# Kernel tuning notes

Hardware: AMD Instinct MI355X
Metric: run time of the kernel (lower is better)

Reference implementation:

```python
import jax, jax.numpy as jnp
import numpy as np

N_HEAD = 16
NEG_BIG = 1e10


def setup_inputs() -> dict:
    key = jax.random.key(0)
    ks = jax.random.split(key, 4)
    B, T, D = 2, 2048, 1024
    x = jax.random.normal(ks[0], (B, T, D), dtype=jnp.float32)
    w_attn = jax.random.normal(ks[1], (D, 3 * D), dtype=jnp.float32) * 0.02
    b_attn = jnp.zeros((3 * D,), dtype=jnp.float32)
    w_proj = jax.random.normal(ks[2], (D, D), dtype=jnp.float32) * 0.02
    b_proj = jnp.zeros((D,), dtype=jnp.float32)
    return {"x": x, "w_attn": w_attn, "b_attn": b_attn, "w_proj": w_proj, "b_proj": b_proj}


def reference(x, w_attn, b_attn, w_proj, b_proj):
    B, T, D = x.shape
    H = N_HEAD
    dh = D // H
    # fused QKV projection (Conv1d == addmm: x @ W + b)
    qkv = x @ w_attn + b_attn                      # [B, T, 3D]
    q, k, v = jnp.split(qkv, 3, axis=-1)
    # split heads -> [B, H, T, dh]
    q = q.reshape(B, T, H, dh).transpose(0, 2, 1, 3)
    k = k.reshape(B, T, H, dh).transpose(0, 2, 1, 3)
    v = v.reshape(B, T, H, dh).transpose(0, 2, 1, 3)
    # scores; repo scales by 1/sqrt(n_head) (its idiosyncrasy, kept faithfully)
    w = jnp.einsum('bhqd,bhkd->bhqk', q, k) / jnp.sqrt(jnp.float32(H))
    # causal mask via repo formula: w*b - 1e10*(1-b), b = tril ones
    b = jnp.tril(jnp.ones((T, T), dtype=w.dtype))
    w = w * b - NEG_BIG * (1.0 - b)
    w = jax.nn.softmax(w, axis=-1)
    a = jnp.einsum('bhqk,bhkd->bhqd', w, v)        # [B, H, T, dh]
    # merge heads
    a = a.transpose(0, 2, 1, 3).reshape(B, T, D)
    a = a @ w_proj + b_proj
    present = jnp.stack([k, v])                     # [2, B, H, T, dh]
    return a, present
```

## Files before the change

kernel.cpp:

```cpp
#include <hip/hip_runtime.h>
#include <hip/hip_bf16.h>

typedef __hip_bfloat16 bf16;
typedef unsigned short ush;
typedef __attribute__((ext_vector_type(8))) short bf16x8;
typedef __attribute__((ext_vector_type(4))) float f32x4;

#define BB 2
#define TT 2048
#define DD 1024
#define HH 16
#define DHH 64
#define MM (BB*TT)
#define N3 (3*DD)

__device__ __forceinline__ bf16  f2b(float x){ return __float2bfloat16(x); }
__device__ __forceinline__ ush   f2bu(float x){ bf16 h = __float2bfloat16(x); return *(ush*)&h; }

#define GLOAD_LDS(gp, lp) \
    __builtin_amdgcn_global_load_lds( \
        (const __attribute__((address_space(1))) void*)(gp), \
        (__attribute__((address_space(3))) void*)(lp), 16, 0, 0)

__global__ __launch_bounds__(256) void prep_fused(
    const float* __restrict__ x, const float* __restrict__ w_attn,
    ush* __restrict__ xbf, ush* __restrict__ wT)
{
    __shared__ ush T[64][68];
    const int tid = threadIdx.x;
    const int bid = blockIdx.x;

    if (bid < 2048) {
        const size_t i = ((size_t)bid * 256 + tid) * 8;
        float4 a = *(const float4*)&x[i];
        float4 b = *(const float4*)&x[i + 4];
        ushort4 u0; u0.x = f2bu(a.x); u0.y = f2bu(a.y); u0.z = f2bu(a.z); u0.w = f2bu(a.w);
        ushort4 u1; u1.x = f2bu(b.x); u1.y = f2bu(b.y); u1.z = f2bu(b.z); u1.w = f2bu(b.w);
        *(ushort4*)&xbf[i] = u0;
        *(ushort4*)&xbf[i + 4] = u1;
        return;
    }
    const int j  = bid - 2048;
    const int c0 = (j % 48) * 64;
    const int r0 = (j / 48) * 64;
    #pragma unroll
    for (int it = 0; it < 4; it++) {
        int idx = it * 256 + tid;
        int i = idx >> 4, jf = idx & 15;
        float4 v = *(const float4*)&w_attn[(size_t)(r0 + i) * N3 + c0 + jf * 4];
        T[jf * 4 + 0][i] = f2bu(v.x);
        T[jf * 4 + 1][i] = f2bu(v.y);
        T[jf * 4 + 2][i] = f2bu(v.z);
        T[jf * 4 + 3][i] = f2bu(v.w);
    }
    __syncthreads();
    #pragma unroll
    for (int it = 0; it < 4; it++) {
        int idx = it * 256 + tid;
        int jj = idx >> 4, i4 = idx & 15;
        *(ushort4*)&wT[(size_t)(c0 + jj) * DD + r0 + i4 * 4] =
            *(const ushort4*)&T[jj][i4 * 4];
    }
}

__global__ __launch_bounds__(256) void transpose_cvt(
    const float* __restrict__ src, ush* __restrict__ dst, int R, int C)
{
    __shared__ ush T[64][68];
    const int tid = threadIdx.x;
    const int c0 = blockIdx.x * 64;
    const int r0 = blockIdx.y * 64;

    #pragma unroll
    for (int it = 0; it < 4; it++) {
        int idx = it * 256 + tid;
        int i = idx >> 4, jf = idx & 15;
        float4 v = *(const float4*)&src[(size_t)(r0 + i) * C + c0 + jf * 4];
        T[jf * 4 + 0][i] = f2bu(v.x);
        T[jf * 4 + 1][i] = f2bu(v.y);
        T[jf * 4 + 2][i] = f2bu(v.z);
        T[jf * 4 + 3][i] = f2bu(v.w);
    }
    __syncthreads();
    #pragma unroll
    for (int it = 0; it < 4; it++) {
        int idx = it * 256 + tid;
        int j = idx >> 4, i4 = idx & 15;
        *(ushort4*)&dst[(size_t)(c0 + j) * R + r0 + i4 * 4] =
            *(const ushort4*)&T[j][i4 * 4];
    }
}

__global__ __launch_bounds__(256) void qkv_mfma(
    const ush* __restrict__ xbf, const ush* __restrict__ wT,
    const float* __restrict__ bias,
    bf16* __restrict__ qws, float* __restrict__ kout, float* __restrict__ vout,
    ush* __restrict__ kbf, ush* __restrict__ vtb, int write_bf)
{
    __shared__ __align__(16) ush As[128 * 32];
    __shared__ __align__(16) ush Bs[128 * 32];

    const int tid  = threadIdx.x;
    const int lane = tid & 63;
    const int w    = tid >> 6;
    const int n16  = lane & 15;
    const int quad = lane >> 4;
    const int row0 = blockIdx.y * 128;
    const int col0 = blockIdx.x * 128;
    const int wrow = (w >> 1) * 64;
    const int wcol = (w & 1) * 64;

    f32x4 acc[4][4];
    #pragma unroll
    for (int mb = 0; mb < 4; mb++)
        #pragma unroll
        for (int nb = 0; nb < 4; nb++) acc[mb][nb] = (f32x4){0.f,0.f,0.f,0.f};

    for (int kk0 = 0; kk0 < DD; kk0 += 32) {
        __syncthreads();
        #pragma unroll
        for (int it = 0; it < 2; it++) {
            int c = it * 256 + tid;
            int r = c >> 2, co = (c & 3) * 8;
            GLOAD_LDS(&xbf[(size_t)(row0 + r) * DD + kk0 + co], &As[c * 8]);
            GLOAD_LDS(&wT[(size_t)(col0 + r) * DD + kk0 + co], &Bs[c * 8]);
        }
        __syncthreads();

        bf16x8 af[4];
        #pragma unroll
        for (int mb = 0; mb < 4; mb++)
            af[mb] = *(const bf16x8*)&As[(wrow + mb * 16 + n16) * 32 + quad * 8];
        #pragma unroll
        for (int nb = 0; nb < 4; nb++) {
            bf16x8 bfr = *(const bf16x8*)&Bs[(wcol + nb * 16 + n16) * 32 + quad * 8];
            #pragma unroll
            for (int mb = 0; mb < 4; mb++)
                acc[mb][nb] = __builtin_amdgcn_mfma_f32_16x16x32_bf16(
                    af[mb], bfr, acc[mb][nb], 0, 0, 0);
        }
    }

    const float qsc = write_bf ? 0.36067376022224085f : 1.0f;

    #pragma unroll
    for (int nb = 0; nb < 4; nb++) {
        const int gc = col0 + wcol + nb * 16 + n16;
        const float bv = bias[gc];
        const int which = gc >> 10;
        const int h = (gc & 1023) >> 6;
        const int d = gc & 63;
        #pragma unroll
        for (int mb = 0; mb < 4; mb++) {
            float vv[4];
            #pragma unroll
            for (int reg = 0; reg < 4; reg++) vv[reg] = acc[mb][nb][reg] + bv;
            const int gr0 = row0 + wrow + mb * 16 + quad * 4;
            const int b_ = gr0 >> 11, t0 = gr0 & 2047;
            const int bh = b_ * HH + h;
            const size_t tbase = ((size_t)bh * TT + t0) * DHH + d;
            if (which == 0) {
                #pragma unroll
                for (int reg = 0; reg < 4; reg++)
                    qws[tbase + (size_t)reg * DHH] = f2b(vv[reg] * qsc);
            } else if (which == 1) {
                if (write_bf) {
                    #pragma unroll
                    for (int reg = 0; reg < 4; reg++)
                        __builtin_nontemporal_store(vv[reg], &kout[tbase + (size_t)reg * DHH]);
                    #pragma unroll
                    for (int reg = 0; reg < 4; reg++)
                        kbf[tbase + (size_t)reg * DHH] = f2bu(vv[reg]);
                } else {
                    #pragma unroll
                    for (int reg = 0; reg < 4; reg++)
                        kout[tbase + (size_t)reg * DHH] = vv[reg];
                }
            } else {
                if (write_bf) {
                    #pragma unroll
                    for (int reg = 0; reg < 4; reg++)
                        __builtin_nontemporal_store(vv[reg], &vout[tbase + (size_t)reg * DHH]);
                    ushort4 u;
                    u.x = f2bu(vv[0]); u.y = f2bu(vv[1]);
                    u.z = f2bu(vv[2]); u.w = f2bu(vv[3]);
                    *(ushort4*)&vtb[((size_t)bh * DHH + d) * TT + t0] = u;
                } else {
                    #pragma unroll
                    for (int reg = 0; reg < 4; reg++)
                        vout[tbase + (size_t)reg * DHH] = vv[reg];
                }
            }
        }
    }
}

__global__ __launch_bounds__(256) void flash_attn_v6(
    const ush* __restrict__ qin, const ush* __restrict__ kbf,
    const ush* __restrict__ vtb, bf16* __restrict__ attn)
{
    __shared__ __align__(16) ush Ks[64][72];
    __shared__ __align__(16) ush Vt[64][72];

    const int tid  = threadIdx.x;
    const int lane = tid & 63;
    const int w    = tid >> 6;
    const int n16  = lane & 15;
    const int quad = lane >> 4;
    const int bh = blockIdx.y;
    const int qi = (bh & 8) ? (31 - (int)blockIdx.x) : (int)blockIdx.x;
    const int q0 = qi * 64;
    const ush* Qb  = qin + (size_t)bh * TT * DHH;
    const ush* Kb  = kbf + (size_t)bh * TT * DHH;
    const ush* Vtb = vtb + (size_t)bh * DHH * TT;
    const int b_ = bh >> 4, h = bh & 15;

    const ush* Qp = Qb + (size_t)(q0 + w * 16 + n16) * DHH + quad * 8;
    const bf16x8 qa0 = *(const bf16x8*)&Qp[0];
    const bf16x8 qa1 = *(const bf16x8*)&Qp[32];

    const int r0c = tid >> 3, c8c = (tid & 7) * 8;
    const int r1c = (256 + tid) >> 3, c8c1 = ((256 + tid) & 7) * 8;

    const int rsb = ((n16 >> 2) << 3) + ((n16 & 1) << 2) + ((n16 & 2) << 4);
    const int rq  = w * 16 + n16;

    bf16x8 kst[2], vst[2];
    {
        const ush* Kp = Kb;
        const ush* Vp = Vtb;
        kst[0] = *(const bf16x8*)&Kp[(size_t)r0c * DHH + c8c];
        kst[1] = *(const bf16x8*)&Kp[(size_t)r1c * DHH + c8c1];
        vst[0] = *(const bf16x8*)&Vp[(size_t)r0c * TT + c8c];
        vst[1] = *(const bf16x8*)&Vp[(size_t)r1c * TT + c8c1];
    }

    f32x4 o[4];
    #pragma unroll
    for (int db = 0; db < 4; db++) o[db] = (f32x4){0.f, 0.f, 0.f, 0.f};
    float lsum = 0.f;

    for (int kt = 0; kt <= qi; kt++) {
        __syncthreads();
        *(bf16x8*)&Ks[r0c][c8c]  = kst[0];
        *(bf16x8*)&Ks[r1c][c8c1] = kst[1];
        *(bf16x8*)&Vt[r0c][c8c]  = vst[0];
        *(bf16x8*)&Vt[r1c][c8c1] = vst[1];
        __syncthreads();

        if (kt < qi) {
            const ush* Kp = Kb + (size_t)((kt + 1) * 64) * DHH;
            const ush* Vp = Vtb + (kt + 1) * 64;
            kst[0] = *(const bf16x8*)&Kp[(size_t)r0c * DHH + c8c];
            kst[1] = *(const bf16x8*)&Kp[(size_t)r1c * DHH + c8c1];
            vst[0] = *(const bf16x8*)&Vp[(size_t)r0c * TT + c8c];
            vst[1] = *(const bf16x8*)&Vp[(size_t)r1c * TT + c8c1];
        }

        f32x4 s[4];
        #pragma unroll
        for (int m = 0; m < 4; m++) {
            bf16x8 kb0 = *(const bf16x8*)&Ks[rsb + m][quad * 8];
            bf16x8 kb1 = *(const bf16x8*)&Ks[rsb + m][32 + quad * 8];
            f32x4 a4 = (f32x4){0.f, 0.f, 0.f, 0.f};
            a4 = __builtin_amdgcn_mfma_f32_16x16x32_bf16(kb0, qa0, a4, 0, 0, 0);
            a4 = __builtin_amdgcn_mfma_f32_16x16x32_bf16(kb1, qa1, a4, 0, 0, 0);
            s[m] = a4;
        }

        float p[4][4];
        if (kt == qi) {
            #pragma unroll
            for (int m = 0; m < 4; m++) {
                #pragma unroll
                for (int reg = 0; reg < 4; reg++) {
                    const int kl = quad * 8 + m + ((reg & 1) << 2) + ((reg >> 1) << 5);
                    float pv = exp2f(s[m][reg]);
                    if (kl > rq) pv = 0.f;
                    p[m][reg] = pv;
                    lsum += pv;
                }
            }
        } else {
            #pragma unroll
            for (int m = 0; m < 4; m++) {
                #pragma unroll
                for (int reg = 0; reg < 4; reg++) {
                    float pv = exp2f(s[m][reg]);
                    p[m][reg] = pv;
                    lsum += pv;
                }
            }
        }

        bf16x8 pa0, pa1;
        #pragma unroll
        for (int m = 0; m < 4; m++) {
            pa0[m]     = (short)f2bu(p[m][0]);
            pa0[m + 4] = (short)f2bu(p[m][1]);
            pa1[m]     = (short)f2bu(p[m][2]);
            pa1[m + 4] = (short)f2bu(p[m][3]);
        }

        #pragma unroll
        for (int db = 0; db < 4; db++) {
            bf16x8 vb0 = *(const bf16x8*)&Vt[db * 16 + n16][quad * 8];
            bf16x8 vb1 = *(const bf16x8*)&Vt[db * 16 + n16][32 + quad * 8];
            o[db] = __builtin_amdgcn_mfma_f32_16x16x32_bf16(pa0, vb0, o[db], 0, 0, 0);
            o[db] = __builtin_amdgcn_mfma_f32_16x16x32_bf16(pa1, vb1, o[db], 0, 0, 0);
        }
    }

    float ls = lsum;
    ls += __shfl_xor(ls, 16);
    ls += __shfl_xor(ls, 32);
    #pragma unroll
    for (int reg = 0; reg < 4; reg++) {
        const float il = 1.0f / __shfl(ls, quad * 4 + reg);
        const int t_ = q0 + w * 16 + quad * 4 + reg;
        bf16* outr = attn + ((size_t)(b_ * TT + t_)) * DD + h * 64 + n16;
        #pragma unroll
        for (int db = 0; db < 4; db++)
            outr[db * 16] = f2b(o[db][reg] * il);
    }
}

__global__ __launch_bounds__(256) void flash_attn_mfma(
    const bf16* __restrict__ qin, const float* __restrict__ kin,
    const float* __restrict__ vin, bf16* __restrict__ attn)
{
    __shared__ __align__(16) ush Qs[64][72];
    __shared__ __align__(16) ush Ks[64][72];
    __shared__ __align__(16) ush Vt[64][72];
    __shared__ __align__(16) ush Ps[4][16][72];

    const int tid  = threadIdx.x;
    const int lane = tid & 63;
    const int w    = tid >> 6;
    const int n16  = lane & 15;
    const int quad = lane >> 4;
    const int qi = blockIdx.x;
    const int bh = blockIdx.y;
    const int q0 = qi * 64;

    const ush*   Qp = (const ush*)qin + ((size_t)bh * TT + q0) * DHH;
    const float* Kb = kin + (size_t)bh * TT * DHH;
    const float* Vb = vin + (size_t)bh * TT * DHH;

    #pragma unroll
    for (int it = 0; it < 4; it++) {
        int idx = (it * 256 + tid) * 4;
        int r = idx >> 6, d = idx & 63;
        *(ushort4*)&Qs[r][d] = *(const ushort4*)&Qp[idx];
    }

    f32x4 o[4];
    #pragma unroll
    for (int db = 0; db < 4; db++) o[db] = (f32x4){0.f, 0.f, 0.f, 0.f};
    float m_old[4] = {-1e30f, -1e30f, -1e30f, -1e30f};
    float l_run[4] = {0.f, 0.f, 0.f, 0.f};

    for (int kt = 0; kt <= qi; kt++) {
        const float* Kp = Kb + (size_t)(kt * 64) * DHH;
        const float* Vp = Vb + (size_t)(kt * 64) * DHH;
        __syncthreads();
        #pragma unroll
        for (int it = 0; it < 4; it++) {
            int idx = (it * 256 + tid) * 4;
            int c = idx >> 6, d = idx & 63;
            float4 kv = *(const float4*)&Kp[idx];
            ushort4 kb;
            kb.x = f2bu(kv.x); kb.y = f2bu(kv.y); kb.z = f2bu(kv.z); kb.w = f2bu(kv.w);
            *(ushort4*)&Ks[c][d] = kb;
        }
        #pragma unroll
        for (int it = 0; it < 4; it++) {
            int c = tid & 63, d0 = (tid >> 6) * 4 + it * 16;
            float4 vv = *(const float4*)&Vp[c * 64 + d0];
            Vt[d0 + 0][c] = f2bu(vv.x);
            Vt[d0 + 1][c] = f2bu(vv.y);
            Vt[d0 + 2][c] = f2bu(vv.z);
            Vt[d0 + 3][c] = f2bu(vv.w);
        }
        __syncthreads();

        bf16x8 qa0 = *(const bf16x8*)&Qs[w * 16 + n16][quad * 8];
        bf16x8 qa1 = *(const bf16x8*)&Qs[w * 16 + n16][32 + quad * 8];
        f32x4 s[4];
        #pragma unroll
        for (int cb = 0; cb < 4; cb++) {
            bf16x8 kb0 = *(const bf16x8*)&Ks[cb * 16 + n16][quad * 8];
            bf16x8 kb1 = *(const bf16x8*)&Ks[cb * 16 + n16][32 + quad * 8];
            f32x4 acc = (f32x4){0.f, 0.f, 0.f, 0.f};
            acc = __builtin_amdgcn_mfma_f32_16x16x32_bf16(qa0, kb0, acc, 0, 0, 0);
            acc = __builtin_amdgcn_mfma_f32_16x16x32_bf16(qa1, kb1, acc, 0, 0, 0);
            s[cb] = acc;
        }

        const int grow_base = q0 + w * 16 + quad * 4;
        const int gcol_base = kt * 64 + n16;
        #pragma unroll
        for (int reg = 0; reg < 4; reg++) {
            float sv[4];
            float pm = -1e30f;
            #pragma unroll
            for (int cb = 0; cb < 4; cb++) {
                float v = s[cb][reg] * 0.25f;
                if (gcol_base + cb * 16 > grow_base + reg) v = -1e10f;
                sv[cb] = v;
                pm = fmaxf(pm, v);
            }
            #pragma unroll
            for (int off = 1; off < 16; off <<= 1)
                pm = fmaxf(pm, __shfl_xor(pm, off));
            float mnew = fmaxf(m_old[reg], pm);
            float alpha = __expf(m_old[reg] - mnew);
            float ps = 0.f;
            #pragma unroll
            for (int cb = 0; cb < 4; cb++) {
                float p = __expf(sv[cb] - mnew);
                Ps[w][quad * 4 + reg][cb * 16 + n16] = f2bu(p);
                ps += p;
            }
            #pragma unroll
            for (int off = 1; off < 16; off <<= 1)
                ps += __shfl_xor(ps, off);
            l_run[reg] = l_run[reg] * alpha + ps;
            m_old[reg] = mnew;
            #pragma unroll
            for (int db = 0; db < 4; db++) o[db][reg] *= alpha;
        }
        __syncthreads();

        bf16x8 pa0 = *(const bf16x8*)&Ps[w][n16][quad * 8];
        bf16x8 pa1 = *(const bf16x8*)&Ps[w][n16][32 + quad * 8];
        #pragma unroll
        for (int db = 0; db < 4; db++) {
            bf16x8 vb0 = *(const bf16x8*)&Vt[db * 16 + n16][quad * 8];
            bf16x8 vb1 = *(const bf16x8*)&Vt[db * 16 + n16][32 + quad * 8];
            o[db] = __builtin_amdgcn_mfma_f32_16x16x32_bf16(pa0, vb0, o[db], 0, 0, 0);
            o[db] = __builtin_amdgcn_mfma_f32_16x16x32_bf16(pa1, vb1, o[db], 0, 0, 0);
        }
    }

    const int b_ = bh >> 4, h = bh & 15;
    #pragma unroll
    for (int reg = 0; reg < 4; reg++) {
        const float il = 1.0f / l_run[reg];
        const int t_ = q0 + w * 16 + quad * 4 + reg;
        bf16* outr = attn + ((size_t)(b_ * TT + t_)) * DD + h * 64 + n16;
        #pragma unroll
        for (int db = 0; db < 4; db++)
            outr[db * 16] = f2b(o[db][reg] * il);
    }
}

__global__ __launch_bounds__(256) void proj_mfma(
    const ush* __restrict__ a, const ush* __restrict__ wpT,
    const float* __restrict__ bias, float* __restrict__ out)
{
    __shared__ __align__(16) ush As[128 * 32];
    __shared__ __align__(16) ush Bs[128 * 32];

    const int tid  = threadIdx.x;
    const int lane = tid & 63;
    const int w    = tid >> 6;
    const int n16  = lane & 15;
    const int quad = lane >> 4;
    const int row0 = blockIdx.y * 128;
    const int col0 = blockIdx.x * 128;
    const int wrow = (w >> 1) * 64;
    const int wcol = (w & 1) * 64;

    f32x4 acc[4][4];
    #pragma unroll
    for (int mb = 0; mb < 4; mb++)
        #pragma unroll
        for (int nb = 0; nb < 4; nb++) acc[mb][nb] = (f32x4){0.f,0.f,0.f,0.f};

    for (int kk0 = 0; kk0 < DD; kk0 += 32) {
        __syncthreads();
        #pragma unroll
        for (int it = 0; it < 2; it++) {
            int c = it * 256 + tid;
            int r = c >> 2, co = (c & 3) * 8;
            GLOAD_LDS(&a[(size_t)(row0 + r) * DD + kk0 + co], &As[c * 8]);
            GLOAD_LDS(&wpT[(size_t)(col0 + r) * DD + kk0 + co], &Bs[c * 8]);
        }
        __syncthreads();

        bf16x8 af[4];
        #pragma unroll
        for (int mb = 0; mb < 4; mb++)
            af[mb] = *(const bf16x8*)&As[(wrow + mb * 16 + n16) * 32 + quad * 8];
        #pragma unroll
        for (int nb = 0; nb < 4; nb++) {
            bf16x8 bfr = *(const bf16x8*)&Bs[(wcol + nb * 16 + n16) * 32 + quad * 8];
            #pragma unroll
            for (int mb = 0; mb < 4; mb++)
                acc[mb][nb] = __builtin_amdgcn_mfma_f32_16x16x32_bf16(
                    af[mb], bfr, acc[mb][nb], 0, 0, 0);
        }
    }

    #pragma unroll
    for (int nb = 0; nb < 4; nb++) {
        const int gc = col0 + wcol + nb * 16 + n16;
        const float bv = bias[gc];
        #pragma unroll
        for (int mb = 0; mb < 4; mb++) {
            #pragma unroll
            for (int reg = 0; reg < 4; reg++) {
                const int gr = row0 + wrow + mb * 16 + quad * 4 + reg;
                __builtin_nontemporal_store(acc[mb][nb][reg] + bv,
                                            &out[(size_t)gr * DD + gc]);
            }
        }
    }
}

extern "C" void kernel_launch(void* const* d_in, const int* in_sizes, int n_in,
                              void* d_out, int out_size, void* d_ws, size_t ws_size,
                              hipStream_t stream) {
    const float *x = nullptr, *w_attn = nullptr, *b_attn = nullptr,
                *w_proj = nullptr, *b_proj = nullptr;
    for (int i = 0; i < n_in; i++) {
        switch (in_sizes[i]) {
            case 4194304: x      = (const float*)d_in[i]; break;
            case 3145728: w_attn = (const float*)d_in[i]; break;
            case 3072:    b_attn = (const float*)d_in[i]; break;
            case 1048576: w_proj = (const float*)d_in[i]; break;
            case 1024:    b_proj = (const float*)d_in[i]; break;
            default: break;
        }
    }
    if (!x || !w_attn || !b_attn || !w_proj || !b_proj) return;

    float* out_a = (float*)d_out;
    float* out_k = out_a + (size_t)MM * DD;
    float* out_v = out_k + (size_t)BB * HH * TT * DHH;

    const size_t MB = 1024 * 1024;
    char* wsc = (char*)d_ws;
    ush*  wT     = (ush*)(wsc + 0);
    bf16* attnws = (bf16*)(wsc + 0);
    bf16* qws    = (bf16*)(wsc + 8 * MB);
    ush*  wpT    = (ush*)(wsc + 8 * MB);
    ush*  xbf    = (ush*)d_out;

    if (ws_size >= 32 * MB) {
        ush* kbf = (ush*)(wsc + 16 * MB);
        ush* vtb = (ush*)(wsc + 24 * MB);
        prep_fused<<<dim3(2048 + 768), 256, 0, stream>>>(x, w_attn, xbf, wT);
        qkv_mfma<<<dim3(N3 / 128, MM / 128), 256, 0, stream>>>(
            xbf, wT, b_attn, qws, out_k, out_v, kbf, vtb, 1);
        flash_attn_v6<<<dim3(TT / 64, BB * HH), 256, 0, stream>>>(
            (const ush*)qws, kbf, vtb, attnws);
        transpose_cvt<<<dim3(DD / 64, DD / 64), 256, 0, stream>>>(w_proj, wpT, DD, DD);
        proj_mfma<<<dim3(DD / 128, MM / 128), 256, 0, stream>>>(
            (const ush*)attnws, wpT, b_proj, out_a);
    } else if (ws_size >= 16 * MB) {
        prep_fused<<<dim3(2048 + 768), 256, 0, stream>>>(x, w_attn, xbf, wT);
        qkv_mfma<<<dim3(N3 / 128, MM / 128), 256, 0, stream>>>(
            xbf, wT, b_attn, qws, out_k, out_v, nullptr, nullptr, 0);
        flash_attn_mfma<<<dim3(TT / 64, BB * HH), 256, 0, stream>>>(
            qws, out_k, out_v, attnws);
        transpose_cvt<<<dim3(DD / 64, DD / 64), 256, 0, stream>>>(w_proj, wpT, DD, DD);
        proj_mfma<<<dim3(DD / 128, MM / 128), 256, 0, stream>>>(
            (const ush*)attnws, wpT, b_proj, out_a);
    }
}
```

Before: 197.6 us.

## Double-buffer K/V tiles in flash attention and narrow projection GEMM tiles

The attention kernel now keeps two LDS buffers for K and V. The next tile is stored while the current one is computed, and the tile after that is prefetched into registers, so each iteration needs one barrier instead of two. The output projection GEMM drops from 128x128 to 128x64 tiles. That doubles the block count from 256 to 512 to fill more CUs, at the cost of more redundant A-tile loads. Its output stores also change from nontemporal to regular stores.

Measured after the change: 194.3 us. Within noise of the previous version (-1.7%).

```diff
diff --git a/kernel.cpp b/kernel.cpp
--- a/kernel.cpp
+++ b/kernel.cpp
@@ -195,12 +195,12 @@
     }
 }
 
-__global__ __launch_bounds__(256) void flash_attn_v6(
+__global__ __launch_bounds__(256) void flash_attn_v7(
     const ush* __restrict__ qin, const ush* __restrict__ kbf,
     const ush* __restrict__ vtb, bf16* __restrict__ attn)
 {
-    __shared__ __align__(16) ush Ks[64][72];
-    __shared__ __align__(16) ush Vt[64][72];
+    __shared__ __align__(16) ush Ks[2][64][72];
+    __shared__ __align__(16) ush Vt[2][64][72];
 
     const int tid  = threadIdx.x;
     const int lane = tid & 63;
@@ -226,42 +226,41 @@
     const int rq  = w * 16 + n16;
 
     bf16x8 kst[2], vst[2];
-    {
-        const ush* Kp = Kb;
-        const ush* Vp = Vtb;
-        kst[0] = *(const bf16x8*)&Kp[(size_t)r0c * DHH + c8c];
-        kst[1] = *(const bf16x8*)&Kp[(size_t)r1c * DHH + c8c1];
-        vst[0] = *(const bf16x8*)&Vp[(size_t)r0c * TT + c8c];
-        vst[1] = *(const bf16x8*)&Vp[(size_t)r1c * TT + c8c1];
-    }
+#define LOAD_TILE(kt) do { \
+        const ush* Kp_ = Kb + (size_t)((kt) * 64) * DHH; \
+        const ush* Vp_ = Vtb + (kt) * 64; \
+        kst[0] = *(const bf16x8*)&Kp_[(size_t)r0c * DHH + c8c]; \
+        kst[1] = *(const bf16x8*)&Kp_[(size_t)r1c * DHH + c8c1]; \
+        vst[0] = *(const bf16x8*)&Vp_[(size_t)r0c * TT + c8c]; \
+        vst[1] = *(const bf16x8*)&Vp_[(size_t)r1c * TT + c8c1]; \
+    } while(0)
+#define STORE_TILE(b) do { \
+        *(bf16x8*)&Ks[b][r0c][c8c]  = kst[0]; \
+        *(bf16x8*)&Ks[b][r1c][c8c1] = kst[1]; \
+        *(bf16x8*)&Vt[b][r0c][c8c]  = vst[0]; \
+        *(bf16x8*)&Vt[b][r1c][c8c1] = vst[1]; \
+    } while(0)
 
     f32x4 o[4];
     #pragma unroll
     for (int db = 0; db < 4; db++) o[db] = (f32x4){0.f, 0.f, 0.f, 0.f};
     float lsum = 0.f;
 
+    LOAD_TILE(0);
+    STORE_TILE(0);
+    if (qi > 0) LOAD_TILE(1);
+    __syncthreads();
+    int c = 0;
+
     for (int kt = 0; kt <= qi; kt++) {
-        __syncthreads();
-        *(bf16x8*)&Ks[r0c][c8c]  = kst[0];
-        *(bf16x8*)&Ks[r1c][c8c1] = kst[1];
-        *(bf16x8*)&Vt[r0c][c8c]  = vst[0];
-        *(bf16x8*)&Vt[r1c][c8c1] = vst[1];
-        __syncthreads();
-
-        if (kt < qi) {
-            const ush* Kp = Kb + (size_t)((kt + 1) * 64) * DHH;
-            const ush* Vp = Vtb + (kt + 1) * 64;
-            kst[0] = *(const bf16x8*)&Kp[(size_t)r0c * DHH + c8c];
-            kst[1] = *(const bf16x8*)&Kp[(size_t)r1c * DHH + c8c1];
-            vst[0] = *(const bf16x8*)&Vp[(size_t)r0c * TT + c8c];
-            vst[1] = *(const bf16x8*)&Vp[(size_t)r1c * TT + c8c1];
-        }
+        if (kt < qi) STORE_TILE(c ^ 1);
+        if (kt + 2 <= qi) LOAD_TILE(kt + 2);
 
         f32x4 s[4];
         #pragma unroll
         for (int m = 0; m < 4; m++) {
-            bf16x8 kb0 = *(const bf16x8*)&Ks[rsb + m][quad * 8];
-            bf16x8 kb1 = *(const bf16x8*)&Ks[rsb + m][32 + quad * 8];
+            bf16x8 kb0 = *(const bf16x8*)&Ks[c][rsb + m][quad * 8];
+            bf16x8 kb1 = *(const bf16x8*)&Ks[c][rsb + m][32 + quad * 8];
             f32x4 a4 = (f32x4){0.f, 0.f, 0.f, 0.f};
             a4 = __builtin_amdgcn_mfma_f32_16x16x32_bf16(kb0, qa0, a4, 0, 0, 0);
             a4 = __builtin_amdgcn_mfma_f32_16x16x32_bf16(kb1, qa1, a4, 0, 0, 0);
@@ -304,11 +303,14 @@
 
         #pragma unroll
         for (int db = 0; db < 4; db++) {
-            bf16x8 vb0 = *(const bf16x8*)&Vt[db * 16 + n16][quad * 8];
-            bf16x8 vb1 = *(const bf16x8*)&Vt[db * 16 + n16][32 + quad * 8];
+            bf16x8 vb0 = *(const bf16x8*)&Vt[c][db * 16 + n16][quad * 8];
+            bf16x8 vb1 = *(const bf16x8*)&Vt[c][db * 16 + n16][32 + quad * 8];
             o[db] = __builtin_amdgcn_mfma_f32_16x16x32_bf16(pa0, vb0, o[db], 0, 0, 0);
             o[db] = __builtin_amdgcn_mfma_f32_16x16x32_bf16(pa1, vb1, o[db], 0, 0, 0);
         }
+
+        __syncthreads();
+        c ^= 1;
     }
 
     float ls = lsum;
@@ -323,6 +325,8 @@
         for (int db = 0; db < 4; db++)
             outr[db * 16] = f2b(o[db][reg] * il);
     }
+#undef LOAD_TILE
+#undef STORE_TILE
 }
 
 __global__ __launch_bounds__(256) void flash_attn_mfma(
@@ -460,7 +464,7 @@
     const float* __restrict__ bias, float* __restrict__ out)
 {
     __shared__ __align__(16) ush As[128 * 32];
-    __shared__ __align__(16) ush Bs[128 * 32];
+    __shared__ __align__(16) ush Bs[64 * 32];
 
     const int tid  = threadIdx.x;
     const int lane = tid & 63;
@@ -468,15 +472,15 @@
     const int n16  = lane & 15;
     const int quad = lane >> 4;
     const int row0 = blockIdx.y * 128;
-    const int col0 = blockIdx.x * 128;
+    const int col0 = blockIdx.x * 64;
     const int wrow = (w >> 1) * 64;
-    const int wcol = (w & 1) * 64;
-
-    f32x4 acc[4][4];
+    const int wcol = (w & 1) * 32;
+
+    f32x4 acc[4][2];
     #pragma unroll
     for (int mb = 0; mb < 4; mb++)
         #pragma unroll
-        for (int nb = 0; nb < 4; nb++) acc[mb][nb] = (f32x4){0.f,0.f,0.f,0.f};
+        for (int nb = 0; nb < 2; nb++) acc[mb][nb] = (f32x4){0.f,0.f,0.f,0.f};
 
     for (int kk0 = 0; kk0 < DD; kk0 += 32) {
         __syncthreads();
@@ -485,7 +489,10 @@
             int c = it * 256 + tid;
             int r = c >> 2, co = (c & 3) * 8;
             GLOAD_LDS(&a[(size_t)(row0 + r) * DD + kk0 + co], &As[c * 8]);
-            GLOAD_LDS(&wpT[(size_t)(col0 + r) * DD + kk0 + co], &Bs[c * 8]);
+        }
+        {
+            int r = tid >> 2, co = (tid & 3) * 8;
+            GLOAD_LDS(&wpT[(size_t)(col0 + r) * DD + kk0 + co], &Bs[tid * 8]);
         }
         __syncthreads();
 
@@ -494,7 +501,7 @@
         for (int mb = 0; mb < 4; mb++)
             af[mb] = *(const bf16x8*)&As[(wrow + mb * 16 + n16) * 32 + quad * 8];
         #pragma unroll
-        for (int nb = 0; nb < 4; nb++) {
+        for (int nb = 0; nb < 2; nb++) {
             bf16x8 bfr = *(const bf16x8*)&Bs[(wcol + nb * 16 + n16) * 32 + quad * 8];
             #pragma unroll
             for (int mb = 0; mb < 4; mb++)
@@ -504,7 +511,7 @@
     }
 
     #pragma unroll
-    for (int nb = 0; nb < 4; nb++) {
+    for (int nb = 0; nb < 2; nb++) {
         const int gc = col0 + wcol + nb * 16 + n16;
         const float bv = bias[gc];
         #pragma unroll
@@ -512,8 +519,7 @@
             #pragma unroll
             for (int reg = 0; reg < 4; reg++) {
                 const int gr = row0 + wrow + mb * 16 + quad * 4 + reg;
-                __builtin_nontemporal_store(acc[mb][nb][reg] + bv,
-                                            &out[(size_t)gr * DD + gc]);
+                out[(size_t)gr * DD + gc] = acc[mb][nb][reg] + bv;
             }
         }
     }
@@ -554,10 +560,10 @@
         prep_fused<<<dim3(2048 + 768), 256, 0, stream>>>(x, w_attn, xbf, wT);
         qkv_mfma<<<dim3(N3 / 128, MM / 128), 256, 0, stream>>>(
             xbf, wT, b_attn, qws, out_k, out_v, kbf, vtb, 1);
-        flash_attn_v6<<<dim3(TT / 64, BB * HH), 256, 0, stream>>>(
+        flash_attn_v7<<<dim3(TT / 64, BB * HH), 256, 0, stream>>>(
             (const ush*)qws, kbf, vtb, attnws);
         transpose_cvt<<<dim3(DD / 64, DD / 64), 256, 0, stream>>>(w_proj, wpT, DD, DD);
-        proj_mfma<<<dim3(DD / 128, MM / 128), 256, 0, stream>>>(
+        proj_mfma<<<dim3(DD / 64, MM / 128), 256, 0, stream>>>(
             (const ush*)attnws, wpT, b_proj, out_a);
     } else if (ws_size >= 16 * MB) {
         prep_fused<<<dim3(2048 + 768), 256, 0, stream>>>(x, w_attn, xbf, wT);
@@ -566,7 +572,7 @@
         flash_attn_mfma<<<dim3(TT / 64, BB * HH), 256, 0, stream>>>(
             qws, out_k, out_v, attnws);
         transpose_cvt<<<dim3(DD / 64, DD / 64), 256, 0, stream>>>(w_proj, wpT, DD, DD);
-        proj_mfma<<<dim3(DD / 128, MM / 128), 256, 0, stream>>>(
+        proj_mfma<<<dim3(DD / 64, MM / 128), 256, 0, stream>>>(
             (const ush*)attnws, wpT, b_proj, out_a);
     }
 }
```
